# Kernel optimization log

Measured on AMD Instinct MI355X. Metric: run time of the kernel, lower is better.

The kernel has to match this reference:

```python
import jax, jax.numpy as jnp
import numpy as np

CTX_SIZE = 4096
LAYER = 1
N_EMBD = 1024
HEAD_SIZE = 64
B, T = 4, 4096


def setup_inputs() -> dict:
    key = jax.random.key(0)
    ks = jax.random.split(key, 4)
    s = 1.0 / np.sqrt(N_EMBD)
    return {
        "x": jax.random.normal(ks[0], (B, T, N_EMBD), dtype=jnp.float32),
        "Wq": jax.random.normal(ks[1], (N_EMBD, HEAD_SIZE), dtype=jnp.float32) * s,
        "bq": jnp.zeros((HEAD_SIZE,), dtype=jnp.float32),
        "Wk": jax.random.normal(ks[2], (N_EMBD, HEAD_SIZE), dtype=jnp.float32) * s,
        "bk": jnp.zeros((HEAD_SIZE,), dtype=jnp.float32),
        "Wv": jax.random.normal(ks[3], (N_EMBD, HEAD_SIZE), dtype=jnp.float32) * s,
        "bv": jnp.zeros((HEAD_SIZE,), dtype=jnp.float32),
    }


def reference(x, Wq, bq, Wk, bk, Wv, bv):
    Bx, Tx, C = x.shape
    t = CTX_SIZE // (2 ** LAYER)
    cut = min(Tx, t)  # static: shapes are concrete under jit

    k = x @ Wk + bk                      # [B, T, H]
    q = x[:, -cut:, :] @ Wq + bq         # [B, cut, H] (fade: queries on last cut tokens)
    v = x @ Wv + bv                      # [B, T, H]

    att = jnp.einsum("bqh,bkh->bqk", q, k) * (C ** -0.5)  # [B, cut, T]

    # row i corresponds to absolute query position (T - cut + i); causal: key j <= that pos
    q_pos = jnp.arange(cut) + (Tx - cut)   # [cut]
    k_pos = jnp.arange(Tx)                 # [T]
    mask = k_pos[None, :] <= q_pos[:, None]  # [cut, T], True = keep
    att = jnp.where(mask[None, :, :], att, -jnp.inf)
    att = jax.nn.softmax(att, axis=-1)
    # dropout p=0.0 (eval mode): identity

    out = jnp.einsum("bqk,bkh->bqh", att, v)  # [B, cut, H]
    return out
```

## Files before the change

### kernel.cpp

```cpp
#include <hip/hip_runtime.h>

#define BB 4
#define TT 4096
#define CUT 2048
#define CE 1024
#define HD 64
#define QSC 0.045084220027780106f

typedef unsigned short u16;
typedef unsigned int u32;
typedef __attribute__((ext_vector_type(8))) short bf16x8;
typedef __attribute__((ext_vector_type(4))) float f32x4;

__device__ __forceinline__ u16 f2b(float f) {
  union { float f; unsigned u; } v; v.f = f;
  unsigned r = v.u + 0x7fffu + ((v.u >> 16) & 1u);
  return (u16)(r >> 16);
}

__device__ __forceinline__ u32 cvtpk(float lo, float hi) {
  u32 r;
  asm("v_cvt_pk_bf16_f32 %0, %1, %2" : "=v"(r) : "v"(lo), "v"(hi));
  return r;
}

__device__ __forceinline__ void gld16(const u16* g, u16* l) {
  __builtin_amdgcn_global_load_lds((const __attribute__((address_space(1))) u32*)g,
                                   (__attribute__((address_space(3))) u32*)l, 16, 0, 0);
}

__global__ void wtrans_k(const float* __restrict__ Wk, const float* __restrict__ Wv,
                         const float* __restrict__ Wq, u16* __restrict__ w3f) {
  int id = blockIdx.x * 256 + threadIdx.x;
  int j    = id & 7;
  int lane = (id >> 3) & 63;
  int f    = id >> 9;
  int kstep = f & 31;
  int mnt   = f >> 5;
  int m  = mnt >> 2;
  int nt = mnt & 3;
  int k   = kstep * 32 + (lane >> 4) * 8 + j;
  int col = nt * 16 + (lane & 15);
  const float* W = (m == 0) ? Wk : (m == 1) ? Wv : Wq;
  w3f[id] = f2b(W[k * 64 + col]);
}

__launch_bounds__(256, 2)
__global__ void proj_k(const float* __restrict__ x, const u16* __restrict__ w3f,
                       const float* __restrict__ bk, const float* __restrict__ bv,
                       const float* __restrict__ bq,
                       u16* __restrict__ KF, u16* __restrict__ VF, u16* __restrict__ Qb) {
  __shared__ u16  st[2][2][12][512];
  __shared__ f32x4 cl[2][12][64];
  const int tid  = threadIdx.x;
  const int lane = tid & 63;
  const int wv   = tid >> 6;
  const int rg   = wv & 1;
  const int kh   = wv >> 1;
  const int l15  = lane & 15;
  const int g    = lane >> 4;
  const int r0   = blockIdx.x * 32;

  f32x4 acc[12];
  #pragma unroll
  for (int t = 0; t < 12; ++t) acc[t] = (f32x4){0.f, 0.f, 0.f, 0.f};

  const float* xrow = x + (size_t)(r0 + rg * 16 + l15) * CE + kh * 512;

  #define STAGE(buf, t)                                                        \
    {                                                                          \
      _Pragma("unroll")                                                        \
      for (int i = 0; i < 6; ++i) {                                            \
        int jj = wv * 6 + i;                                                   \
        int hh = jj / 12, mm = jj % 12;                                        \
        gld16(&w3f[(size_t)(mm * 32 + hh * 16 + (t)) * 512 + lane * 8],        \
              &st[buf][hh][mm][0]);                                            \
      }                                                                        \
    }

  f32x4 xs[2][2];
  xs[0][0] = *(const f32x4*)(xrow + g * 8);
  xs[0][1] = *(const f32x4*)(xrow + g * 8 + 4);
  STAGE(0, 0);
  asm volatile("s_waitcnt vmcnt(0)" ::: "memory");
  __syncthreads();

  #pragma unroll
  for (int t = 0; t < 16; ++t) {
    const int cur = t & 1, nxt = cur ^ 1;
    if (t < 15) {
      STAGE(nxt, t + 1);
      const float* xp = xrow + (t + 1) * 32 + g * 8;
      xs[nxt][0] = *(const f32x4*)xp;
      xs[nxt][1] = *(const f32x4*)(xp + 4);
    }
    bf16x8 a;
    #pragma unroll
    for (int j = 0; j < 4; ++j) {
      a[j]     = (short)f2b(xs[cur][0][j]);
      a[j + 4] = (short)f2b(xs[cur][1][j]);
    }
    #pragma unroll
    for (int mnt = 0; mnt < 12; ++mnt) {
      bf16x8 bfr = *(const bf16x8*)&st[cur][kh][mnt][lane * 8];
      acc[mnt] = __builtin_amdgcn_mfma_f32_16x16x32_bf16(a, bfr, acc[mnt], 0, 0, 0);
    }
    asm volatile("s_waitcnt vmcnt(0)" ::: "memory");
    __syncthreads();
  }
  #undef STAGE

  if (kh == 1) {
    #pragma unroll
    for (int t = 0; t < 12; ++t) cl[rg][t][lane] = acc[t];
  }
  __syncthreads();
  if (kh == 0) {
    #pragma unroll
    for (int t = 0; t < 12; ++t) acc[t] += cl[rg][t][lane];

    const int b    = r0 >> 12;
    const int cch  = (r0 >> 6) & 63;
    const int half = (r0 >> 5) & 1;
    const int h    = rg;

    const int t0 = r0 & (TT - 1);
    if (t0 >= CUT) {
      const int trow = t0 - CUT + h * 16;
      #pragma unroll
      for (int nt = 0; nt < 4; ++nt) {
        int col = nt * 16 + l15;
        float bc = bq[col];
        #pragma unroll
        for (int r = 0; r < 4; ++r)
          Qb[((size_t)b * CUT + trow + g * 4 + r) * HD + col] =
              f2b((acc[8 + nt][r] + bc) * QSC);
      }
    }
    {
      u16* KFc = KF + ((size_t)(b * 64 + cch) * 8) * 512;
      const int kt2 = (half * 2 + h) * 2;
      #pragma unroll
      for (int nt = 0; nt < 4; ++nt) {
        int col = nt * 16 + l15;
        float bc = bk[col];
        f32x4 v = acc[nt];
        const int off = (kt2 + (nt >> 1)) * 512 + 128 * ((nt & 1) * 2 + (l15 >> 3)) + (l15 & 7);
        #pragma unroll
        for (int r = 0; r < 4; ++r)
          KFc[off + (g * 4 + r) * 8] = f2b(v[r] + bc);
      }
    }
    {
      u16* VFc = VF + ((size_t)(b * 64 + cch) * 8) * 512;
      #pragma unroll
      for (int nt = 0; nt < 4; ++nt) {
        int col = nt * 16 + l15;
        float bc = bv[col];
        f32x4 v = acc[4 + nt];
        #pragma unroll
        for (int r = 0; r < 4; ++r) {
          int tt = h * 16 + g * 4 + r;
          VFc[(half * 4 + nt) * 512 + (l15 + 16 * (tt >> 3)) * 8 + (tt & 7)] = f2b(v[r] + bc);
        }
      }
    }
  }
}

__launch_bounds__(512, 4)
__global__ void attn_k(const u16* __restrict__ Qb, const u16* __restrict__ KF,
                       const u16* __restrict__ VF, float* __restrict__ out) {
  __shared__ u32   PLd[8][16][36];
  __shared__ float OO[8][16][66];
  __shared__ float OL[8][16];
  const int tid  = threadIdx.x;
  const int lane = tid & 63;
  const int wv   = tid >> 6;
  const int l15  = lane & 15;
  const int g    = lane >> 4;
  const int id   = blockIdx.x;
  const int b    = id & 3;
  const int i0   = (id >> 2) * 16;

  const int qabs = CUT + i0 + l15;
  const int qmin = CUT + i0;

  const u16* qrow = Qb + ((size_t)b * CUT + i0 + l15) * HD;
  bf16x8 qf0 = *(const bf16x8*)&qrow[g * 8];
  bf16x8 qf1 = *(const bf16x8*)&qrow[32 + g * 8];

  f32x4 o[4];
  #pragma unroll
  for (int dt = 0; dt < 4; ++dt) o[dt] = (f32x4){0.f, 0.f, 0.f, 0.f};
  float lsum = 0.f;

  const int kv_end = CUT + i0 + 16;
  const int nch = (kv_end + 63) >> 6;
  const u16* KFb = KF + (size_t)b * 64 * 8 * 512;
  const u16* VFb = VF + (size_t)b * 64 * 8 * 512;

  for (int c = wv; c < nch; c += 8) {
    const int kv0 = c << 6;

    const u16* kp = KFb + (size_t)c * 4096 + lane * 8;
    bf16x8 ka[4][2];
    #pragma unroll
    for (int kt = 0; kt < 4; ++kt) {
      ka[kt][0] = *(const bf16x8*)(kp + (kt * 2 + 0) * 512);
      ka[kt][1] = *(const bf16x8*)(kp + (kt * 2 + 1) * 512);
    }
    const u16* vp = VFb + (size_t)c * 4096 + lane * 8;
    bf16x8 va[2][4];
    #pragma unroll
    for (int c2 = 0; c2 < 2; ++c2)
      #pragma unroll
      for (int dt = 0; dt < 4; ++dt)
        va[c2][dt] = *(const bf16x8*)(vp + (c2 * 4 + dt) * 512);

    f32x4 st[4];
    __builtin_amdgcn_s_setprio(1);
    #pragma unroll
    for (int kt = 0; kt < 4; ++kt) {
      f32x4 s = (f32x4){0.f, 0.f, 0.f, 0.f};
      s = __builtin_amdgcn_mfma_f32_16x16x32_bf16(ka[kt][0], qf0, s, 0, 0, 0);
      s = __builtin_amdgcn_mfma_f32_16x16x32_bf16(ka[kt][1], qf1, s, 0, 0, 0);
      st[kt] = s;
    }
    __builtin_amdgcn_s_setprio(0);

    if (kv0 + 63 <= qmin) {
      #pragma unroll
      for (int kt = 0; kt < 4; ++kt)
        #pragma unroll
        for (int r = 0; r < 4; ++r) {
          float p = exp2f(st[kt][r]);
          st[kt][r] = p;
          lsum += p;
        }
    } else {
      #pragma unroll
      for (int kt = 0; kt < 4; ++kt)
        #pragma unroll
        for (int r = 0; r < 4; ++r) {
          int key = kv0 + kt * 16 + g * 4 + r;
          float p = exp2f(st[kt][r]);
          p = (key <= qabs) ? p : 0.f;
          st[kt][r] = p;
          lsum += p;
        }
    }

    #pragma unroll
    for (int kt = 0; kt < 4; ++kt) {
      u32 d0 = cvtpk(st[kt][0], st[kt][1]);
      u32 d1 = cvtpk(st[kt][2], st[kt][3]);
      u32* p = &PLd[wv][l15][kt * 8 + g * 2];
      p[0] = d0; p[1] = d1;
    }

    __builtin_amdgcn_s_setprio(1);
    #pragma unroll
    for (int c2 = 0; c2 < 2; ++c2) {
      bf16x8 pa = *(const bf16x8*)&PLd[wv][l15][c2 * 16 + g * 4];
      #pragma unroll
      for (int dt = 0; dt < 4; ++dt)
        o[dt] = __builtin_amdgcn_mfma_f32_16x16x32_bf16(pa, va[c2][dt], o[dt], 0, 0, 0);
    }
    __builtin_amdgcn_s_setprio(0);
  }

  lsum += __shfl_xor(lsum, 16);
  lsum += __shfl_xor(lsum, 32);
  if (lane < 16) OL[wv][l15] = lsum;
  #pragma unroll
  for (int dt = 0; dt < 4; ++dt)
    #pragma unroll
    for (int r = 0; r < 4; ++r)
      OO[wv][g * 4 + r][dt * 16 + l15] = o[dt][r];
  __syncthreads();

  #pragma unroll
  for (int e = tid; e < 1024; e += 512) {
    int q = e >> 6, d = e & 63;
    float L = 0.f, O = 0.f;
    #pragma unroll
    for (int w = 0; w < 8; ++w) { L += OL[w][q]; O += OO[w][q][d]; }
    out[((size_t)b * CUT + i0 + q) * HD + d] = O / L;
  }
}

extern "C" void kernel_launch(void* const* d_in, const int* in_sizes, int n_in,
                              void* d_out, int out_size, void* d_ws, size_t ws_size,
                              hipStream_t stream) {
  const float* x  = (const float*)d_in[0];
  const float* Wq = (const float*)d_in[1];
  const float* bq = (const float*)d_in[2];
  const float* Wk = (const float*)d_in[3];
  const float* bk = (const float*)d_in[4];
  const float* Wv = (const float*)d_in[5];
  const float* bv = (const float*)d_in[6];
  float* out = (float*)d_out;

  u16* Qb  = (u16*)d_ws;
  u16* W3F = Qb + (size_t)BB * CUT * HD;
  u16* KF  = W3F + (size_t)384 * 512;
  u16* VF  = KF + (size_t)BB * 64 * 8 * 512;

  wtrans_k<<<768, 256, 0, stream>>>(Wk, Wv, Wq, W3F);
  proj_k<<<512, 256, 0, stream>>>(x, W3F, bk, bv, bq, KF, VF, Qb);
  attn_k<<<512, 512, 0, stream>>>(Qb, KF, VF, out);
}
```

Baseline: 50.15 us.

## Process 32 queries per attention block and prefetch next K chunk

Each attention block now handles two 16-row query tiles, so every K/V chunk loaded from global memory is reused across 32 queries and the grid is halved. The K fragments for the next chunk are loaded ahead of use into registers, to hide global-load latency behind the current chunk's MFMAs. This raises register pressure (launch bounds lowered to 2 blocks per CU) and halves the number of blocks, which could reduce occupancy and load balance across CUs. The final reduction is done in two phases with extra barriers so the shared buffer can be reused.

```diff
diff --git a/kernel.cpp b/kernel.cpp
--- a/kernel.cpp
+++ b/kernel.cpp
@@ -168,12 +168,12 @@
   }
 }
 
-__launch_bounds__(512, 4)
+__launch_bounds__(512, 2)
 __global__ void attn_k(const u16* __restrict__ Qb, const u16* __restrict__ KF,
                        const u16* __restrict__ VF, float* __restrict__ out) {
   __shared__ u32   PLd[8][16][36];
   __shared__ float OO[8][16][66];
-  __shared__ float OL[8][16];
+  __shared__ float OL[8][32];
   const int tid  = threadIdx.x;
   const int lane = tid & 63;
   const int wv   = tid >> 6;
@@ -181,35 +181,42 @@
   const int g    = lane >> 4;
   const int id   = blockIdx.x;
   const int b    = id & 3;
-  const int i0   = (id >> 2) * 16;
-
-  const int qabs = CUT + i0 + l15;
+  const int i0   = (id >> 2) * 32;
+
   const int qmin = CUT + i0;
 
-  const u16* qrow = Qb + ((size_t)b * CUT + i0 + l15) * HD;
-  bf16x8 qf0 = *(const bf16x8*)&qrow[g * 8];
-  bf16x8 qf1 = *(const bf16x8*)&qrow[32 + g * 8];
-
-  f32x4 o[4];
-  #pragma unroll
-  for (int dt = 0; dt < 4; ++dt) o[dt] = (f32x4){0.f, 0.f, 0.f, 0.f};
-  float lsum = 0.f;
-
-  const int kv_end = CUT + i0 + 16;
-  const int nch = (kv_end + 63) >> 6;
+  bf16x8 qf[2][2];
+  #pragma unroll
+  for (int h = 0; h < 2; ++h) {
+    const u16* qrow = Qb + ((size_t)b * CUT + i0 + h * 16 + l15) * HD;
+    qf[h][0] = *(const bf16x8*)&qrow[g * 8];
+    qf[h][1] = *(const bf16x8*)&qrow[32 + g * 8];
+  }
+
+  f32x4 o[2][4];
+  #pragma unroll
+  for (int h = 0; h < 2; ++h)
+    #pragma unroll
+    for (int dt = 0; dt < 4; ++dt) o[h][dt] = (f32x4){0.f, 0.f, 0.f, 0.f};
+  float lsum[2] = {0.f, 0.f};
+
+  const int nch = (CUT + i0 + 32 + 63) >> 6;
   const u16* KFb = KF + (size_t)b * 64 * 8 * 512;
   const u16* VFb = VF + (size_t)b * 64 * 8 * 512;
 
-  for (int c = wv; c < nch; c += 8) {
-    const int kv0 = c << 6;
-
-    const u16* kp = KFb + (size_t)c * 4096 + lane * 8;
-    bf16x8 ka[4][2];
+  bf16x8 ka[4][2];
+  {
+    const u16* kp = KFb + (size_t)wv * 4096 + lane * 8;
     #pragma unroll
     for (int kt = 0; kt < 4; ++kt) {
       ka[kt][0] = *(const bf16x8*)(kp + (kt * 2 + 0) * 512);
       ka[kt][1] = *(const bf16x8*)(kp + (kt * 2 + 1) * 512);
     }
+  }
+
+  for (int c = wv; c < nch; c += 8) {
+    const int kv0 = c << 6;
+
     const u16* vp = VFb + (size_t)c * 4096 + lane * 8;
     bf16x8 va[2][4];
     #pragma unroll
@@ -218,75 +225,110 @@
       for (int dt = 0; dt < 4; ++dt)
         va[c2][dt] = *(const bf16x8*)(vp + (c2 * 4 + dt) * 512);
 
-    f32x4 st[4];
+    bf16x8 kb[4][2];
+    const int cn = c + 8;
+    if (cn < nch) {
+      const u16* kp = KFb + (size_t)cn * 4096 + lane * 8;
+      #pragma unroll
+      for (int kt = 0; kt < 4; ++kt) {
+        kb[kt][0] = *(const bf16x8*)(kp + (kt * 2 + 0) * 512);
+        kb[kt][1] = *(const bf16x8*)(kp + (kt * 2 + 1) * 512);
+      }
+    }
+
+    f32x4 st[2][4];
     __builtin_amdgcn_s_setprio(1);
     #pragma unroll
-    for (int kt = 0; kt < 4; ++kt) {
-      f32x4 s = (f32x4){0.f, 0.f, 0.f, 0.f};
-      s = __builtin_amdgcn_mfma_f32_16x16x32_bf16(ka[kt][0], qf0, s, 0, 0, 0);
-      s = __builtin_amdgcn_mfma_f32_16x16x32_bf16(ka[kt][1], qf1, s, 0, 0, 0);
-      st[kt] = s;
-    }
+    for (int h = 0; h < 2; ++h)
+      #pragma unroll
+      for (int kt = 0; kt < 4; ++kt) {
+        f32x4 s = (f32x4){0.f, 0.f, 0.f, 0.f};
+        s = __builtin_amdgcn_mfma_f32_16x16x32_bf16(ka[kt][0], qf[h][0], s, 0, 0, 0);
+        s = __builtin_amdgcn_mfma_f32_16x16x32_bf16(ka[kt][1], qf[h][1], s, 0, 0, 0);
+        st[h][kt] = s;
+      }
     __builtin_amdgcn_s_setprio(0);
 
-    if (kv0 + 63 <= qmin) {
-      #pragma unroll
-      for (int kt = 0; kt < 4; ++kt)
-        #pragma unroll
-        for (int r = 0; r < 4; ++r) {
-          float p = exp2f(st[kt][r]);
-          st[kt][r] = p;
-          lsum += p;
-        }
-    } else {
-      #pragma unroll
-      for (int kt = 0; kt < 4; ++kt)
-        #pragma unroll
-        for (int r = 0; r < 4; ++r) {
-          int key = kv0 + kt * 16 + g * 4 + r;
-          float p = exp2f(st[kt][r]);
-          p = (key <= qabs) ? p : 0.f;
-          st[kt][r] = p;
-          lsum += p;
-        }
-    }
-
-    #pragma unroll
-    for (int kt = 0; kt < 4; ++kt) {
-      u32 d0 = cvtpk(st[kt][0], st[kt][1]);
-      u32 d1 = cvtpk(st[kt][2], st[kt][3]);
-      u32* p = &PLd[wv][l15][kt * 8 + g * 2];
-      p[0] = d0; p[1] = d1;
-    }
-
-    __builtin_amdgcn_s_setprio(1);
-    #pragma unroll
-    for (int c2 = 0; c2 < 2; ++c2) {
-      bf16x8 pa = *(const bf16x8*)&PLd[wv][l15][c2 * 16 + g * 4];
-      #pragma unroll
-      for (int dt = 0; dt < 4; ++dt)
-        o[dt] = __builtin_amdgcn_mfma_f32_16x16x32_bf16(pa, va[c2][dt], o[dt], 0, 0, 0);
-    }
-    __builtin_amdgcn_s_setprio(0);
-  }
-
-  lsum += __shfl_xor(lsum, 16);
-  lsum += __shfl_xor(lsum, 32);
-  if (lane < 16) OL[wv][l15] = lsum;
-  #pragma unroll
-  for (int dt = 0; dt < 4; ++dt)
-    #pragma unroll
-    for (int r = 0; r < 4; ++r)
-      OO[wv][g * 4 + r][dt * 16 + l15] = o[dt][r];
-  __syncthreads();
-
-  #pragma unroll
-  for (int e = tid; e < 1024; e += 512) {
-    int q = e >> 6, d = e & 63;
-    float L = 0.f, O = 0.f;
-    #pragma unroll
-    for (int w = 0; w < 8; ++w) { L += OL[w][q]; O += OO[w][q][d]; }
-    out[((size_t)b * CUT + i0 + q) * HD + d] = O / L;
+    #pragma unroll
+    for (int h = 0; h < 2; ++h) {
+      if (kv0 + 63 <= qmin + h * 16) {
+        #pragma unroll
+        for (int kt = 0; kt < 4; ++kt)
+          #pragma unroll
+          for (int r = 0; r < 4; ++r) {
+            float p = exp2f(st[h][kt][r]);
+            st[h][kt][r] = p;
+            lsum[h] += p;
+          }
+      } else {
+        const int qabs = qmin + h * 16 + l15;
+        #pragma unroll
+        for (int kt = 0; kt < 4; ++kt)
+          #pragma unroll
+          for (int r = 0; r < 4; ++r) {
+            int key = kv0 + kt * 16 + g * 4 + r;
+            float p = exp2f(st[h][kt][r]);
+            p = (key <= qabs) ? p : 0.f;
+            st[h][kt][r] = p;
+            lsum[h] += p;
+          }
+      }
+    }
+
+    #pragma unroll
+    for (int h = 0; h < 2; ++h) {
+      #pragma unroll
+      for (int kt = 0; kt < 4; ++kt) {
+        u32 d0 = cvtpk(st[h][kt][0], st[h][kt][1]);
+        u32 d1 = cvtpk(st[h][kt][2], st[h][kt][3]);
+        u32* p = &PLd[wv][l15][kt * 8 + g * 2];
+        p[0] = d0; p[1] = d1;
+      }
+      __builtin_amdgcn_s_setprio(1);
+      #pragma unroll
+      for (int c2 = 0; c2 < 2; ++c2) {
+        bf16x8 pa = *(const bf16x8*)&PLd[wv][l15][c2 * 16 + g * 4];
+        #pragma unroll
+        for (int dt = 0; dt < 4; ++dt)
+          o[h][dt] = __builtin_amdgcn_mfma_f32_16x16x32_bf16(pa, va[c2][dt], o[h][dt], 0, 0, 0);
+      }
+      __builtin_amdgcn_s_setprio(0);
+    }
+
+    if (cn < nch) {
+      #pragma unroll
+      for (int kt = 0; kt < 4; ++kt) {
+        ka[kt][0] = kb[kt][0];
+        ka[kt][1] = kb[kt][1];
+      }
+    }
+  }
+
+  #pragma unroll
+  for (int h = 0; h < 2; ++h) {
+    float ls = lsum[h];
+    ls += __shfl_xor(ls, 16);
+    ls += __shfl_xor(ls, 32);
+    if (lane < 16) OL[wv][h * 16 + l15] = ls;
+  }
+
+  #pragma unroll
+  for (int ph = 0; ph < 2; ++ph) {
+    #pragma unroll
+    for (int dt = 0; dt < 4; ++dt)
+      #pragma unroll
+      for (int r = 0; r < 4; ++r)
+        OO[wv][g * 4 + r][dt * 16 + l15] = o[ph][dt][r];
+    __syncthreads();
+    #pragma unroll
+    for (int e = tid; e < 1024; e += 512) {
+      int q = e >> 6, d = e & 63;
+      float L = 0.f, O = 0.f;
+      #pragma unroll
+      for (int w = 0; w < 8; ++w) { L += OL[w][ph * 16 + q]; O += OO[w][q][d]; }
+      out[((size_t)b * CUT + i0 + ph * 16 + q) * HD + d] = O / L;
+    }
+    __syncthreads();
   }
 }
 
@@ -309,5 +351,5 @@
 
   wtrans_k<<<768, 256, 0, stream>>>(Wk, Wv, Wq, W3F);
   proj_k<<<512, 256, 0, stream>>>(x, W3F, bk, bv, bq, KF, VF, Qb);
-  attn_k<<<512, 512, 0, stream>>>(Qb, KF, VF, out);
-}
+  attn_k<<<256, 512, 0, stream>>>(Qb, KF, VF, out);
+}
```

After: 50.99 us. About the same (+1.7%).

## Share K/V tiles across 128-query blocks via LDS and split-KV combine

Applied to the files above, without the earlier changes.

The attention kernel now has each block handle 128 queries (16 per wave) and split the KV range four ways across blocks. K/V chunks are staged through double-buffered LDS with async loads, so all eight waves reuse them instead of each wave reading its own chunk from global memory. Partial outputs and row sums go to a workspace and are reduced by a new combine kernel. The projection kernel's pipelining is also reworked, using sched barriers and a partial vmcnt wait so the next stage's loads stay in flight. This trades a fourth kernel launch and extra partial-result traffic for far less redundant K/V loading, with only 256 attention blocks in flight.

```diff
diff --git a/kernel.cpp b/kernel.cpp
--- a/kernel.cpp
+++ b/kernel.cpp
@@ -79,20 +79,23 @@
     }
 
   f32x4 xs[2][2];
+  STAGE(0, 0);
+  __builtin_amdgcn_sched_barrier(0);
   xs[0][0] = *(const f32x4*)(xrow + g * 8);
   xs[0][1] = *(const f32x4*)(xrow + g * 8 + 4);
-  STAGE(0, 0);
   asm volatile("s_waitcnt vmcnt(0)" ::: "memory");
-  __syncthreads();
+  __builtin_amdgcn_s_barrier();
 
   #pragma unroll
   for (int t = 0; t < 16; ++t) {
     const int cur = t & 1, nxt = cur ^ 1;
     if (t < 15) {
       STAGE(nxt, t + 1);
+      __builtin_amdgcn_sched_barrier(0);
       const float* xp = xrow + (t + 1) * 32 + g * 8;
       xs[nxt][0] = *(const f32x4*)xp;
       xs[nxt][1] = *(const f32x4*)(xp + 4);
+      __builtin_amdgcn_sched_barrier(0);
     }
     bf16x8 a;
     #pragma unroll
@@ -105,8 +108,12 @@
       bf16x8 bfr = *(const bf16x8*)&st[cur][kh][mnt][lane * 8];
       acc[mnt] = __builtin_amdgcn_mfma_f32_16x16x32_bf16(a, bfr, acc[mnt], 0, 0, 0);
     }
-    asm volatile("s_waitcnt vmcnt(0)" ::: "memory");
-    __syncthreads();
+    if (t < 15) {
+      asm volatile("s_waitcnt vmcnt(2)" ::: "memory");
+    } else {
+      asm volatile("s_waitcnt vmcnt(0)" ::: "memory");
+    }
+    __builtin_amdgcn_s_barrier();
   }
   #undef STAGE
 
@@ -168,12 +175,12 @@
   }
 }
 
-__launch_bounds__(512, 4)
+__launch_bounds__(512)
 __global__ void attn_k(const u16* __restrict__ Qb, const u16* __restrict__ KF,
-                       const u16* __restrict__ VF, float* __restrict__ out) {
-  __shared__ u32   PLd[8][16][36];
-  __shared__ float OO[8][16][66];
-  __shared__ float OL[8][16];
+                       const u16* __restrict__ VF, float* __restrict__ OP,
+                       float* __restrict__ LP) {
+  __shared__ u16 kv[2][16][512];
+  __shared__ u32 PLd[8][16][36];
   const int tid  = threadIdx.x;
   const int lane = tid & 63;
   const int wv   = tid >> 6;
@@ -181,12 +188,14 @@
   const int g    = lane >> 4;
   const int id   = blockIdx.x;
   const int b    = id & 3;
-  const int i0   = (id >> 2) * 16;
-
-  const int qabs = CUT + i0 + l15;
-  const int qmin = CUT + i0;
-
-  const u16* qrow = Qb + ((size_t)b * CUT + i0 + l15) * HD;
+  const int kvs  = (id >> 2) & 3;
+  const int tile = id >> 4;
+  const int i0   = tile * 128;
+
+  const int qmin = CUT + i0 + wv * 16;
+  const int qabs = qmin + l15;
+
+  const u16* qrow = Qb + ((size_t)b * CUT + i0 + wv * 16 + l15) * HD;
   bf16x8 qf0 = *(const bf16x8*)&qrow[g * 8];
   bf16x8 qf1 = *(const bf16x8*)&qrow[32 + g * 8];
 
@@ -195,36 +204,41 @@
   for (int dt = 0; dt < 4; ++dt) o[dt] = (f32x4){0.f, 0.f, 0.f, 0.f};
   float lsum = 0.f;
 
-  const int kv_end = CUT + i0 + 16;
-  const int nch = (kv_end + 63) >> 6;
+  const int nch = (CUT + i0 + 128) >> 6;
   const u16* KFb = KF + (size_t)b * 64 * 8 * 512;
   const u16* VFb = VF + (size_t)b * 64 * 8 * 512;
 
-  for (int c = wv; c < nch; c += 8) {
+  #define ASTAGE(buf, c)                                                       \
+    {                                                                          \
+      _Pragma("unroll")                                                        \
+      for (int i = 0; i < 2; ++i) {                                            \
+        int f = wv * 2 + i;                                                    \
+        const u16* src = (f < 8)                                               \
+            ? &KFb[(size_t)(c) * 4096 + f * 512 + lane * 8]                    \
+            : &VFb[(size_t)(c) * 4096 + (f - 8) * 512 + lane * 8];             \
+        gld16(src, &kv[buf][f][0]);                                            \
+      }                                                                        \
+    }
+
+  ASTAGE(0, kvs);
+  asm volatile("s_waitcnt vmcnt(0)" ::: "memory");
+  __builtin_amdgcn_s_barrier();
+
+  int cur = 0;
+  for (int c = kvs; c < nch; c += 4) {
     const int kv0 = c << 6;
-
-    const u16* kp = KFb + (size_t)c * 4096 + lane * 8;
-    bf16x8 ka[4][2];
-    #pragma unroll
-    for (int kt = 0; kt < 4; ++kt) {
-      ka[kt][0] = *(const bf16x8*)(kp + (kt * 2 + 0) * 512);
-      ka[kt][1] = *(const bf16x8*)(kp + (kt * 2 + 1) * 512);
-    }
-    const u16* vp = VFb + (size_t)c * 4096 + lane * 8;
-    bf16x8 va[2][4];
-    #pragma unroll
-    for (int c2 = 0; c2 < 2; ++c2)
-      #pragma unroll
-      for (int dt = 0; dt < 4; ++dt)
-        va[c2][dt] = *(const bf16x8*)(vp + (c2 * 4 + dt) * 512);
+    const int cn = c + 4;
+    if (cn < nch) ASTAGE(cur ^ 1, cn);
 
     f32x4 st[4];
     __builtin_amdgcn_s_setprio(1);
     #pragma unroll
     for (int kt = 0; kt < 4; ++kt) {
+      bf16x8 kf0 = *(const bf16x8*)&kv[cur][kt * 2 + 0][lane * 8];
+      bf16x8 kf1 = *(const bf16x8*)&kv[cur][kt * 2 + 1][lane * 8];
       f32x4 s = (f32x4){0.f, 0.f, 0.f, 0.f};
-      s = __builtin_amdgcn_mfma_f32_16x16x32_bf16(ka[kt][0], qf0, s, 0, 0, 0);
-      s = __builtin_amdgcn_mfma_f32_16x16x32_bf16(ka[kt][1], qf1, s, 0, 0, 0);
+      s = __builtin_amdgcn_mfma_f32_16x16x32_bf16(kf0, qf0, s, 0, 0, 0);
+      s = __builtin_amdgcn_mfma_f32_16x16x32_bf16(kf1, qf1, s, 0, 0, 0);
       st[kt] = s;
     }
     __builtin_amdgcn_s_setprio(0);
@@ -264,30 +278,45 @@
     for (int c2 = 0; c2 < 2; ++c2) {
       bf16x8 pa = *(const bf16x8*)&PLd[wv][l15][c2 * 16 + g * 4];
       #pragma unroll
-      for (int dt = 0; dt < 4; ++dt)
-        o[dt] = __builtin_amdgcn_mfma_f32_16x16x32_bf16(pa, va[c2][dt], o[dt], 0, 0, 0);
+      for (int dt = 0; dt < 4; ++dt) {
+        bf16x8 vf = *(const bf16x8*)&kv[cur][8 + c2 * 4 + dt][lane * 8];
+        o[dt] = __builtin_amdgcn_mfma_f32_16x16x32_bf16(pa, vf, o[dt], 0, 0, 0);
+      }
     }
     __builtin_amdgcn_s_setprio(0);
-  }
+
+    asm volatile("s_waitcnt vmcnt(0)" ::: "memory");
+    __builtin_amdgcn_s_barrier();
+    cur ^= 1;
+  }
+  #undef ASTAGE
 
   lsum += __shfl_xor(lsum, 16);
   lsum += __shfl_xor(lsum, 32);
-  if (lane < 16) OL[wv][l15] = lsum;
+  float* OPb = OP + (size_t)id * 128 * 64;
   #pragma unroll
   for (int dt = 0; dt < 4; ++dt)
     #pragma unroll
     for (int r = 0; r < 4; ++r)
-      OO[wv][g * 4 + r][dt * 16 + l15] = o[dt][r];
-  __syncthreads();
-
-  #pragma unroll
-  for (int e = tid; e < 1024; e += 512) {
-    int q = e >> 6, d = e & 63;
-    float L = 0.f, O = 0.f;
-    #pragma unroll
-    for (int w = 0; w < 8; ++w) { L += OL[w][q]; O += OO[w][q][d]; }
-    out[((size_t)b * CUT + i0 + q) * HD + d] = O / L;
-  }
+      OPb[(wv * 16 + g * 4 + r) * 64 + dt * 16 + l15] = o[dt][r];
+  if (lane < 16) LP[(size_t)id * 128 + wv * 16 + l15] = lsum;
+}
+
+__global__ void comb_k(const float* __restrict__ OP, const float* __restrict__ LP,
+                       float* __restrict__ out) {
+  int id = blockIdx.x * 256 + threadIdx.x;
+  int d    = id & 63;
+  int row  = (id >> 6) & 127;
+  int tile = (id >> 13) & 15;
+  int b    = id >> 17;
+  float O = 0.f, L = 0.f;
+  #pragma unroll
+  for (int s = 0; s < 4; ++s) {
+    int bid = tile * 16 + s * 4 + b;
+    O += OP[(size_t)bid * 8192 + row * 64 + d];
+    L += LP[(size_t)bid * 128 + row];
+  }
+  out[((size_t)b * CUT + tile * 128 + row) * HD + d] = O / L;
 }
 
 extern "C" void kernel_launch(void* const* d_in, const int* in_sizes, int n_in,
@@ -306,8 +335,11 @@
   u16* W3F = Qb + (size_t)BB * CUT * HD;
   u16* KF  = W3F + (size_t)384 * 512;
   u16* VF  = KF + (size_t)BB * 64 * 8 * 512;
+  float* OP = (float*)(VF + (size_t)BB * 64 * 8 * 512);
+  float* LP = OP + (size_t)256 * 128 * 64;
 
   wtrans_k<<<768, 256, 0, stream>>>(Wk, Wv, Wq, W3F);
   proj_k<<<512, 256, 0, stream>>>(x, W3F, bk, bv, bq, KF, VF, Qb);
-  attn_k<<<512, 512, 0, stream>>>(Qb, KF, VF, out);
-}
+  attn_k<<<256, 512, 0, stream>>>(Qb, KF, VF, OP, LP);
+  comb_k<<<2048, 256, 0, stream>>>(OP, LP, out);
+}
```

Measured after the change: 56.76 us. 13.2% more time.
